# Optimization experiments

Measured on AMD Instinct MI355X. Metric: run time of the kernel, lower is better.

Reference implementation:

```python
import jax, jax.numpy as jnp
import numpy as np

N = 50000          # nodes
E = 400000         # edges
MUL0 = 16          # multiplicity of 0e irreps (node & message)
MUL1 = 8           # multiplicity of 1o irreps
RBF = 8
HID = 64
CUTOFF = 5.0
WNUM = MUL0*MUL0 + MUL1*MUL0 + MUL0*MUL1 + MUL1*MUL1  # 576 tp weights per edge
EPS = 1e-8
INV_SQRT3 = 1.0 / np.sqrt(3.0).astype(np.float32)
A_PATH = 1.0 / np.sqrt(float(MUL0 + MUL1))  # e3nn path normalization (fan_in = 24 for both outputs)


def _split_sv(x):
    # x: [n, 40] -> scalars [n,16], vectors [n,8,3]
    return x[:, :MUL0], x[:, MUL0:].reshape(-1, MUL1, 3)


def _irrep_norm(x):
    # RMS-normalize each irrep block separately (IrrepNorm)
    s, v = _split_sv(x)
    s_rms = jnp.sqrt(jnp.mean(s * s, axis=-1, keepdims=True) + EPS)
    v_rms = jnp.sqrt(jnp.mean(jnp.sum(v * v, axis=-1), axis=-1, keepdims=True) + EPS)
    return jnp.concatenate([s / s_rms, (v / v_rms[:, :, None]).reshape(-1, MUL1 * 3)], axis=-1)


def setup_inputs() -> dict:
    key = jax.random.key(0)
    ks = jax.random.split(key, 20)
    inp = {
        'x': jax.random.normal(ks[0], (N, MUL0 + 3 * MUL1), jnp.float32),
        'edge_src': jax.random.randint(ks[1], (E,), 0, N, jnp.int32),
        'edge_dst': jax.random.randint(ks[2], (E,), 0, N, jnp.int32),
        'edge_sh': jax.random.normal(ks[3], (E, 4), jnp.float32),
        'edge_rbf': jax.random.uniform(ks[4], (E, RBF), jnp.float32),
        'edge_len': jax.random.uniform(ks[5], (E,), jnp.float32) * CUTOFF,
        # radial MLP producing per-edge TP weights
        'w_r1': jax.random.normal(ks[6], (RBF, HID), jnp.float32) / np.sqrt(RBF),
        'b_r1': jnp.zeros((HID,), jnp.float32),
        'w_r2': jax.random.normal(ks[7], (HID, WNUM), jnp.float32) / np.sqrt(HID),
        'b_r2': jnp.zeros((WNUM,), jnp.float32),
        # edge gate MLP
        'w_g1': jax.random.normal(ks[8], (RBF, HID), jnp.float32) / np.sqrt(RBF),
        'b_g1': jnp.zeros((HID,), jnp.float32),
        'w_g2': jax.random.normal(ks[9], (HID, 1), jnp.float32) / np.sqrt(HID),
        'b_g2': jnp.zeros((1,), jnp.float32),
        # msg_linear: 16x0e+8x1o -> (16x0e scalars + 8x0e gates) + 8x1o gated
        'Wm_s': jax.random.normal(ks[10], (MUL0, MUL0 + MUL1), jnp.float32),
        'Wm_v': jax.random.normal(ks[11], (MUL1, MUL1), jnp.float32),
        # update_linear and self_linear: 16x0e+8x1o -> 16x0e+8x1o
        'Wu_s': jax.random.normal(ks[12], (MUL0, MUL0), jnp.float32),
        'Wu_v': jax.random.normal(ks[13], (MUL1, MUL1), jnp.float32),
        'Ws_s': jax.random.normal(ks[14], (MUL0, MUL0), jnp.float32),
        'Ws_v': jax.random.normal(ks[15], (MUL1, MUL1), jnp.float32),
        'res_scale': jnp.asarray(0.1, jnp.float32),
    }
    return inp


def reference(x, edge_src, edge_dst, edge_sh, edge_rbf, edge_len,
              w_r1, b_r1, w_r2, b_r2, w_g1, b_g1, w_g2, b_g2,
              Wm_s, Wm_v, Wu_s, Wu_v, Ws_s, Ws_v, res_scale):
    x_norm = _irrep_norm(x)
    xs, xv = _split_sv(x_norm)

    # per-edge TP weights from radial MLP
    w = jax.nn.silu(edge_rbf @ w_r1 + b_r1) @ w_r2 + b_r2            # [E, 576]
    o = MUL0 * MUL0
    w1 = w[:, :o].reshape(-1, MUL0, MUL0)                            # 0e x 0e -> 0e
    w2 = w[:, o:o + MUL1 * MUL0].reshape(-1, MUL1, MUL0)             # 1o x 1o -> 0e
    o += MUL1 * MUL0
    w3 = w[:, o:o + MUL0 * MUL1].reshape(-1, MUL0, MUL1)             # 0e x 1o -> 1o
    o += MUL0 * MUL1
    w4 = w[:, o:].reshape(-1, MUL1, MUL1)                            # 1o x 0e -> 1o

    # gather per-edge source features
    s_e = xs[edge_src]                                               # [E,16]
    v_e = xv[edge_src]                                               # [E,8,3]
    sh0 = edge_sh[:, :1]                                             # [E,1]
    sh1 = edge_sh[:, 1:4]                                            # [E,3]

    # fully-connected tensor product (CG for l<=1, component norm, path norm)
    m0 = A_PATH * (jnp.einsum('ei,eij->ej', s_e * sh0, w1)
                   + INV_SQRT3 * jnp.einsum('eic,ec,eij->ej', v_e, sh1, w2))   # [E,16]
    m1 = A_PATH * (jnp.einsum('ei,eij,ec->ejc', s_e, w3, sh1)
                   + jnp.einsum('eic,eij->ejc', v_e * sh0[:, :, None], w4))    # [E,8,3]

    # cutoff and sigmoid edge gate
    cw = 0.5 * (jnp.cos(jnp.pi * edge_len / CUTOFF) + 1.0) * (edge_len < CUTOFF)
    gw = jax.nn.sigmoid(jax.nn.silu(edge_rbf @ w_g1 + b_g1) @ w_g2 + b_g2)     # [E,1]
    ew = cw[:, None] * gw                                                      # [E,1]
    m0 = m0 * ew
    m1 = m1 * ew[:, :, None]

    # scatter-add into destination nodes, normalize by total edge weight
    agg0 = jax.ops.segment_sum(m0, edge_dst, num_segments=N)                   # [N,16]
    agg1 = jax.ops.segment_sum(m1.reshape(-1, MUL1 * 3), edge_dst, num_segments=N).reshape(-1, MUL1, 3)
    norm = jax.ops.segment_sum(ew, edge_dst, num_segments=N)                   # [N,1]
    norm = jnp.maximum(norm, EPS)
    agg0 = agg0 / norm
    agg1 = agg1 / norm[:, :, None]

    # msg_linear (equivariant linear, fan-in normalized)
    sc = agg0 @ Wm_s / np.sqrt(MUL0)                                           # [N,24]
    vv = jnp.einsum('nic,ij->njc', agg1, Wm_v) / np.sqrt(MUL1)                 # [N,8,3]

    # gated nonlinearity
    scal = jax.nn.silu(sc[:, :MUL0])
    gates = jax.nn.sigmoid(sc[:, MUL0:])
    vg = vv * gates[:, :, None]

    # update + self interaction, residual
    out_s = scal @ Wu_s / np.sqrt(MUL0) + xs @ Ws_s / np.sqrt(MUL0)
    out_v = (jnp.einsum('nic,ij->njc', vg, Wu_v) + jnp.einsum('nic,ij->njc', xv, Ws_v)) / np.sqrt(MUL1)
    out = jnp.concatenate([out_s, out_v.reshape(-1, MUL1 * 3)], axis=-1)
    return x + res_scale * out
```

## Files before the change

### kernel.cpp

```cpp
#include <hip/hip_runtime.h>
#include <cstdint>

#define MUL0 16
#define MUL1 8
#define NRBF 8
#define HID 64
#define WNUM 576
#define CUTOFF 5.0f
#define EPSF 1e-8f

#define INV_SQRT3 0.57735026918962576f
#define A_PATH    0.20412414523193154f
#define Q16       0.25f
#define Q8        0.35355339059327373f
#define PI_OVER_CUT 0.62831853071795865f

typedef _Float16 f16;
typedef _Float16 f16x8 __attribute__((ext_vector_type(8)));
typedef float f32x4 __attribute__((ext_vector_type(4)));

__device__ __forceinline__ float sigm(float x) { return 1.0f / (1.0f + __expf(-x)); }

extern "C" __global__ __launch_bounds__(256) void k_prep_w2t(
    const float* __restrict__ w_r2, f16* __restrict__ W2T) {
  int t = blockIdx.x * 256 + threadIdx.x;
  if (t >= HID * WNUM) return;
  int n = t >> 6, k = t & 63;
  W2T[n * 64 + k] = (f16)w_r2[k * WNUM + n];
}

extern "C" __global__ __launch_bounds__(64) void k_xnorm(
    const float* __restrict__ x, float* __restrict__ xnorm, int N) {
  int n = blockIdx.x * 64 + threadIdx.x;
  if (n >= N) return;
  const float4* xr = (const float4*)(x + (long long)n * 40);
  float4 vv[10];
#pragma unroll
  for (int i = 0; i < 10; i++) vv[i] = xr[i];
  float* f = (float*)vv;
  float ss = 0.f, vs = 0.f;
#pragma unroll
  for (int i = 0; i < 16; i++) ss += f[i] * f[i];
#pragma unroll
  for (int i = 16; i < 40; i++) vs += f[i] * f[i];
  float sr = rsqrtf(ss * (1.0f / 16.0f) + EPSF);
  float vr = rsqrtf(vs * (1.0f / 8.0f) + EPSF);
#pragma unroll
  for (int i = 0; i < 16; i++) f[i] *= sr;
#pragma unroll
  for (int i = 16; i < 40; i++) f[i] *= vr;
  float4* o = (float4*)(xnorm + (long long)n * 40);
#pragma unroll
  for (int i = 0; i < 10; i++) o[i] = vv[i];
}

extern "C" __global__ __launch_bounds__(256) void k_hist(
    const int* __restrict__ edst, int* __restrict__ hist, int E) {
  int e = blockIdx.x * 256 + threadIdx.x;
  if (e < E) atomicAdd(&hist[edst[e]], 1);
}

extern "C" __global__ __launch_bounds__(256) void k_scan1(
    const int* __restrict__ hist, int* __restrict__ iscan,
    int* __restrict__ bsum, int N) {
  __shared__ int sm[256];
  int i = blockIdx.x * 256 + threadIdx.x;
  int t = threadIdx.x;
  sm[t] = (i < N) ? hist[i] : 0;
  __syncthreads();
#pragma unroll
  for (int d = 1; d < 256; d <<= 1) {
    int add = (t >= d) ? sm[t - d] : 0;
    __syncthreads();
    sm[t] += add;
    __syncthreads();
  }
  if (i < N) iscan[i] = sm[t];
  if (t == 255) bsum[blockIdx.x] = sm[255];
}

extern "C" __global__ __launch_bounds__(256) void k_scan2(
    int* __restrict__ bsum, int nb) {
  __shared__ int sm[256];
  int t = threadIdx.x;
  sm[t] = (t < nb) ? bsum[t] : 0;
  __syncthreads();
#pragma unroll
  for (int d = 1; d < 256; d <<= 1) {
    int add = (t >= d) ? sm[t - d] : 0;
    __syncthreads();
    sm[t] += add;
    __syncthreads();
  }
  if (t < nb) bsum[t] = sm[t];
}

extern "C" __global__ __launch_bounds__(256) void k_scan3(
    const int* __restrict__ hist, const int* __restrict__ iscan,
    const int* __restrict__ bsum, int* __restrict__ cursor, int N) {
  int i = blockIdx.x * 256 + threadIdx.x;
  if (i >= N) return;
  int base = blockIdx.x ? bsum[blockIdx.x - 1] : 0;
  cursor[i] = iscan[i] - hist[i] + base;
}

extern "C" __global__ __launch_bounds__(256) void k_scatter(
    const int* __restrict__ edst, int* __restrict__ cursor,
    int* __restrict__ perm, int E) {
  int e = blockIdx.x * 256 + threadIdx.x;
  if (e >= E) return;
  int p = atomicAdd(&cursor[edst[e]], 1);
  perm[p] = e;
}

extern "C" __global__ __launch_bounds__(256, 3) void k_edge(
    const float* __restrict__ xnorm, const int* __restrict__ perm,
    const int* __restrict__ esrc, const int* __restrict__ edst,
    const float* __restrict__ sh, const float* __restrict__ rbf,
    const float* __restrict__ elen,
    const float* __restrict__ w_r1, const float* __restrict__ b_r1,
    const float* __restrict__ w_g1, const float* __restrict__ b_g1,
    const float* __restrict__ w_g2, const float* __restrict__ b_g2,
    const float* __restrict__ b_r2, const f16* __restrict__ W2T,
    float* __restrict__ agg0, float* __restrict__ agg1,
    float* __restrict__ normb, int E) {
  __shared__ __align__(16) f16   s_H[4][32][72];
  __shared__ __align__(16) float s_sn[4][32][20];
  __shared__ __align__(16) float s_v[4][32][24];
  __shared__ __align__(16) float s_a1[4][32][12];
  __shared__ __align__(16) float s_sh[4][32][4];
  __shared__ __align__(16) float s_rbf[4][32][8];

  const int t = threadIdx.x;
  const int w = t >> 6;
  const int lane = t & 63;
  const long long eb = (long long)blockIdx.x * 128 + w * 32;

  int pl = 0, dstv = 0, srcv = 0;
  float lenv = 1e9f;
  if (lane < 32) {
    long long g2 = eb + lane;
    if (g2 < E) pl = perm[g2];
    srcv = esrc[pl];
    dstv = edst[pl];
    lenv = elen[pl];
    *(float4*)&s_sh[w][lane][0] = *(const float4*)&sh[(long long)pl * 4];
  }
  {
    int e = lane >> 1, half = lane & 1;
    int pe = __shfl(pl, e);
    *(float4*)&s_rbf[w][e][half * 4] =
        *(const float4*)&rbf[(long long)pe * 8 + half * 4];
  }
  __syncthreads();

  {
    const int ge_l = lane >> 2;
    const int part = lane & 3;
#pragma unroll
    for (int g = 0; g < 2; g++) {
      int e = g * 16 + ge_l;
      int srcn = __shfl(srcv, e);
      const float* xr = xnorm + (long long)srcn * 40;
      if (part < 2) {
        float4 aLo = *(const float4*)(xr + part * 8);
        float4 aHi = *(const float4*)(xr + part * 8 + 4);
        *(float4*)&s_sn[w][e][part * 8] = aLo;
        *(float4*)&s_sn[w][e][part * 8 + 4] = aHi;
      } else {
        const int i0 = (part - 2) * 4;
        const float* vp = xr + 16 + i0 * 3;
        float4 v0 = *(const float4*)(vp);
        float4 v1 = *(const float4*)(vp + 4);
        float4 v2 = *(const float4*)(vp + 8);
        *(float4*)&s_v[w][e][i0 * 3] = v0;
        *(float4*)&s_v[w][e][i0 * 3 + 4] = v1;
        *(float4*)&s_v[w][e][i0 * 3 + 8] = v2;
        float4 shq = *(const float4*)&s_sh[w][e][0];
        float s1x = shq.y, s1y = shq.z, s1z = shq.w;
        s_a1[w][e][i0]     = INV_SQRT3 * (v0.x * s1x + v0.y * s1y + v0.z * s1z);
        s_a1[w][e][i0 + 1] = INV_SQRT3 * (v0.w * s1x + v1.x * s1y + v1.y * s1z);
        s_a1[w][e][i0 + 2] = INV_SQRT3 * (v1.z * s1x + v1.w * s1y + v2.x * s1z);
        s_a1[w][e][i0 + 3] = INV_SQRT3 * (v2.y * s1x + v2.z * s1y + v2.w * s1z);
      }
    }
  }

  {
    float wr[8];
#pragma unroll
    for (int r = 0; r < 8; r++) wr[r] = w_r1[r * HID + lane];
    float bh = b_r1[lane];
#pragma unroll 4
    for (int u = 0; u < 32; u++) {
      float4 ra = *(const float4*)&s_rbf[w][u][0];
      float4 rb = *(const float4*)&s_rbf[w][u][4];
      float acc = bh + ra.x * wr[0] + ra.y * wr[1] + ra.z * wr[2] + ra.w * wr[3]
                     + rb.x * wr[4] + rb.y * wr[5] + rb.z * wr[6] + rb.w * wr[7];
      s_H[w][u][lane] = (f16)(acc * sigm(acc));
    }
  }

  float ewv = 0.f;
  {
    const int eg = lane & 31;
    const int hf = lane >> 5;
    float4 ga = *(const float4*)&s_rbf[w][eg][0];
    float4 gb = *(const float4*)&s_rbf[w][eg][4];
    float rv[8] = {ga.x, ga.y, ga.z, ga.w, gb.x, gb.y, gb.z, gb.w};
    float accp = 0.f;
#pragma unroll
    for (int ch = 0; ch < 2; ch++) {
      const int base = hf * 32 + ch * 16;
      float ttv[16];
      {
        const float4 b0 = *(const float4*)&b_g1[base];
        const float4 b1 = *(const float4*)&b_g1[base + 4];
        const float4 b2 = *(const float4*)&b_g1[base + 8];
        const float4 b3 = *(const float4*)&b_g1[base + 12];
        ttv[0] = b0.x; ttv[1] = b0.y; ttv[2] = b0.z; ttv[3] = b0.w;
        ttv[4] = b1.x; ttv[5] = b1.y; ttv[6] = b1.z; ttv[7] = b1.w;
        ttv[8] = b2.x; ttv[9] = b2.y; ttv[10] = b2.z; ttv[11] = b2.w;
        ttv[12] = b3.x; ttv[13] = b3.y; ttv[14] = b3.z; ttv[15] = b3.w;
      }
#pragma unroll
      for (int r = 0; r < 8; r++) {
        const float* wg = w_g1 + r * HID + base;
        float4 w0 = *(const float4*)(wg);
        float4 w1 = *(const float4*)(wg + 4);
        float4 w2 = *(const float4*)(wg + 8);
        float4 w3 = *(const float4*)(wg + 12);
        float rr = rv[r];
        ttv[0] += rr * w0.x; ttv[1] += rr * w0.y; ttv[2] += rr * w0.z; ttv[3] += rr * w0.w;
        ttv[4] += rr * w1.x; ttv[5] += rr * w1.y; ttv[6] += rr * w1.z; ttv[7] += rr * w1.w;
        ttv[8] += rr * w2.x; ttv[9] += rr * w2.y; ttv[10] += rr * w2.z; ttv[11] += rr * w2.w;
        ttv[12] += rr * w3.x; ttv[13] += rr * w3.y; ttv[14] += rr * w3.z; ttv[15] += rr * w3.w;
      }
      const float4 g0 = *(const float4*)&w_g2[base];
      const float4 g1 = *(const float4*)&w_g2[base + 4];
      const float4 g2 = *(const float4*)&w_g2[base + 8];
      const float4 g3 = *(const float4*)&w_g2[base + 12];
      float gw[16] = {g0.x, g0.y, g0.z, g0.w, g1.x, g1.y, g1.z, g1.w,
                      g2.x, g2.y, g2.z, g2.w, g3.x, g3.y, g3.z, g3.w};
#pragma unroll
      for (int k = 0; k < 16; k++) accp += ttv[k] * sigm(ttv[k]) * gw[k];
    }
    accp += __shfl_xor(accp, 32);
    if (lane < 32) {
      long long g2e = eb + lane;
      if (g2e < E) {
        float len = lenv;
        float cw = (len < CUTOFF) ? 0.5f * (__cosf(PI_OVER_CUT * len) + 1.0f) : 0.f;
        ewv = cw * sigm(accp + b_g2[0]);
      }
    }
  }
  __syncthreads();

  const int quad = lane >> 4;
  const int c = lane & 15;

  const f16x8 af00 = *(const f16x8*)&s_H[w][c][quad * 8];
  const f16x8 af01 = *(const f16x8*)&s_H[w][c][32 + quad * 8];
  const f16x8 af10 = *(const f16x8*)&s_H[w][16 + c][quad * 8];
  const f16x8 af11 = *(const f16x8*)&s_H[w][16 + c][32 + quad * 8];

  float p1[2][4] = {{0.f}}, p2[2][4] = {{0.f}}, t3[2][4] = {{0.f}};
  float mx[2][4] = {{0.f}}, my[2][4] = {{0.f}}, mz[2][4] = {{0.f}};

  const f16* wb = W2T + (long long)c * 64 + quad * 8;
  const float* bp = b_r2 + c;

#pragma unroll 2
  for (int jt = 0; jt < 16; jt++) {
    f16x8 b0 = *(const f16x8*)(wb + jt * 1024);
    f16x8 b1 = *(const f16x8*)(wb + jt * 1024 + 32);
    float bias = bp[jt * 16];
    f32x4 C0 = {0.f, 0.f, 0.f, 0.f};
    C0 = __builtin_amdgcn_mfma_f32_16x16x32_f16(af00, b0, C0, 0, 0, 0);
    C0 = __builtin_amdgcn_mfma_f32_16x16x32_f16(af01, b1, C0, 0, 0, 0);
    f32x4 C1 = {0.f, 0.f, 0.f, 0.f};
    C1 = __builtin_amdgcn_mfma_f32_16x16x32_f16(af10, b0, C1, 0, 0, 0);
    C1 = __builtin_amdgcn_mfma_f32_16x16x32_f16(af11, b1, C1, 0, 0, 0);
#pragma unroll
    for (int r = 0; r < 4; r++) {
      p1[0][r] += s_sn[w][quad * 4 + r][jt] * (C0[r] + bias);
      p1[1][r] += s_sn[w][16 + quad * 4 + r][jt] * (C1[r] + bias);
    }
  }
#pragma unroll 2
  for (int jt = 16; jt < 24; jt++) {
    f16x8 b0 = *(const f16x8*)(wb + jt * 1024);
    f16x8 b1 = *(const f16x8*)(wb + jt * 1024 + 32);
    float bias = bp[jt * 16];
    f32x4 C0 = {0.f, 0.f, 0.f, 0.f};
    C0 = __builtin_amdgcn_mfma_f32_16x16x32_f16(af00, b0, C0, 0, 0, 0);
    C0 = __builtin_amdgcn_mfma_f32_16x16x32_f16(af01, b1, C0, 0, 0, 0);
    f32x4 C1 = {0.f, 0.f, 0.f, 0.f};
    C1 = __builtin_amdgcn_mfma_f32_16x16x32_f16(af10, b0, C1, 0, 0, 0);
    C1 = __builtin_amdgcn_mfma_f32_16x16x32_f16(af11, b1, C1, 0, 0, 0);
    const int i = jt - 16;
#pragma unroll
    for (int r = 0; r < 4; r++) {
      p2[0][r] += s_a1[w][quad * 4 + r][i] * (C0[r] + bias);
      p2[1][r] += s_a1[w][16 + quad * 4 + r][i] * (C1[r] + bias);
    }
  }
#pragma unroll 2
  for (int jt = 24; jt < 32; jt++) {
    f16x8 b0 = *(const f16x8*)(wb + jt * 1024);
    f16x8 b1 = *(const f16x8*)(wb + jt * 1024 + 32);
    float bias = bp[jt * 16];
    f32x4 C0 = {0.f, 0.f, 0.f, 0.f};
    C0 = __builtin_amdgcn_mfma_f32_16x16x32_f16(af00, b0, C0, 0, 0, 0);
    C0 = __builtin_amdgcn_mfma_f32_16x16x32_f16(af01, b1, C0, 0, 0, 0);
    f32x4 C1 = {0.f, 0.f, 0.f, 0.f};
    C1 = __builtin_amdgcn_mfma_f32_16x16x32_f16(af10, b0, C1, 0, 0, 0);
    C1 = __builtin_amdgcn_mfma_f32_16x16x32_f16(af11, b1, C1, 0, 0, 0);
    const int i = (jt - 24) * 2 + (c >> 3);
#pragma unroll
    for (int r = 0; r < 4; r++) {
      t3[0][r] += s_sn[w][quad * 4 + r][i] * (C0[r] + bias);
      t3[1][r] += s_sn[w][16 + quad * 4 + r][i] * (C1[r] + bias);
    }
  }
#pragma unroll 2
  for (int jt = 32; jt < 36; jt++) {
    f16x8 b0 = *(const f16x8*)(wb + jt * 1024);
    f16x8 b1 = *(const f16x8*)(wb + jt * 1024 + 32);
    float bias = bp[jt * 16];
    f32x4 C0 = {0.f, 0.f, 0.f, 0.f};
    C0 = __builtin_amdgcn_mfma_f32_16x16x32_f16(af00, b0, C0, 0, 0, 0);
    C0 = __builtin_amdgcn_mfma_f32_16x16x32_f16(af01, b1, C0, 0, 0, 0);
    f32x4 C1 = {0.f, 0.f, 0.f, 0.f};
    C1 = __builtin_amdgcn_mfma_f32_16x16x32_f16(af10, b0, C1, 0, 0, 0);
    C1 = __builtin_amdgcn_mfma_f32_16x16x32_f16(af11, b1, C1, 0, 0, 0);
    const int i = (jt - 32) * 2 + (c >> 3);
#pragma unroll
    for (int r = 0; r < 4; r++) {
      float wv0 = C0[r] + bias;
      float wv1 = C1[r] + bias;
      mx[0][r] += s_v[w][quad * 4 + r][3 * i] * wv0;
      my[0][r] += s_v[w][quad * 4 + r][3 * i + 1] * wv0;
      mz[0][r] += s_v[w][quad * 4 + r][3 * i + 2] * wv0;
      mx[1][r] += s_v[w][16 + quad * 4 + r][3 * i] * wv1;
      my[1][r] += s_v[w][16 + quad * 4 + r][3 * i + 1] * wv1;
      mz[1][r] += s_v[w][16 + quad * 4 + r][3 * i + 2] * wv1;
    }
  }

#pragma unroll
  for (int g = 0; g < 2; g++)
#pragma unroll
    for (int r = 0; r < 4; r++) {
      t3[g][r] += __shfl_xor(t3[g][r], 8);
      mx[g][r] += __shfl_xor(mx[g][r], 8);
      my[g][r] += __shfl_xor(my[g][r], 8);
      mz[g][r] += __shfl_xor(mz[g][r], 8);
    }

#pragma unroll
  for (int g = 0; g < 2; g++) {
    const int e0g = g * 16 + quad * 4;
    int cur = __shfl(dstv, e0g);
    float acc0 = 0.f, a1x = 0.f, a1y = 0.f, a1z = 0.f, nacc = 0.f;
#pragma unroll
    for (int r = 0; r < 4; r++) {
      const int e = e0g + r;
      const int dst = __shfl(dstv, e);
      const float ew = __shfl(ewv, e);
      if (dst != cur) {
        atomicAdd(&agg0[(long long)cur * 16 + c], acc0);
        if (c < 8) {
          long long b = (long long)cur * 24 + (long long)c * 3;
          atomicAdd(&agg1[b], a1x);
          atomicAdd(&agg1[b + 1], a1y);
          atomicAdd(&agg1[b + 2], a1z);
        } else if (c == 8) {
          atomicAdd(&normb[cur], nacc);
        }
        acc0 = a1x = a1y = a1z = nacc = 0.f;
        cur = dst;
      }
      float sc = A_PATH * ew;
      float sh0 = s_sh[w][e][0];
      acc0 += (sh0 * p1[g][r] + p2[g][r]) * sc;
      if (c < 8) {
        float t3v = t3[g][r] * sc;
        float scs = sc * sh0;
        a1x += t3v * s_sh[w][e][1] + mx[g][r] * scs;
        a1y += t3v * s_sh[w][e][2] + my[g][r] * scs;
        a1z += t3v * s_sh[w][e][3] + mz[g][r] * scs;
      } else if (c == 8) {
        nacc += ew;
      }
    }
    atomicAdd(&agg0[(long long)cur * 16 + c], acc0);
    if (c < 8) {
      long long b = (long long)cur * 24 + (long long)c * 3;
      atomicAdd(&agg1[b], a1x);
      atomicAdd(&agg1[b + 1], a1y);
      atomicAdd(&agg1[b + 2], a1z);
    } else if (c == 8) {
      atomicAdd(&normb[cur], nacc);
    }
  }
}

extern "C" __global__ __launch_bounds__(64) void k_node(
    const float* __restrict__ x, const float* __restrict__ xnorm,
    const float* __restrict__ agg0, const float* __restrict__ agg1,
    const float* __restrict__ normb, const float* __restrict__ Wm_s,
    const float* __restrict__ Wm_v, const float* __restrict__ Wu_s,
    const float* __restrict__ Wu_v, const float* __restrict__ Ws_s,
    const float* __restrict__ Ws_v, const float* __restrict__ res_scale_p,
    float* __restrict__ out, int N) {
  __shared__ float sWms[384];
  __shared__ float sWmv[64];
  __shared__ float sWus[256];
  __shared__ float sWuv[64];
  __shared__ float sWss[256];
  __shared__ float sWsv[64];
  int t = threadIdx.x;
  for (int i = t; i < 384; i += 64) sWms[i] = Wm_s[i];
  sWmv[t] = Wm_v[t];
  for (int i = t; i < 256; i += 64) sWus[i] = Wu_s[i];
  sWuv[t] = Wu_v[t];
  for (int i = t; i < 256; i += 64) sWss[i] = Ws_s[i];
  sWsv[t] = Ws_v[t];
  __syncthreads();
  int n = blockIdx.x * 64 + t;
  if (n >= N) return;

  float inv = 1.0f / fmaxf(normb[n], EPSF);
  float4 a04[4], a14[6];
  {
    const float4* p = (const float4*)(agg0 + (long long)n * 16);
#pragma unroll
    for (int i = 0; i < 4; i++) a04[i] = p[i];
    const float4* q = (const float4*)(agg1 + (long long)n * 24);
#pragma unroll
    for (int i = 0; i < 6; i++) a14[i] = q[i];
  }
  float* a0 = (float*)a04;
  float* a1 = (float*)a14;
#pragma unroll
  for (int i = 0; i < 16; i++) a0[i] *= inv;
#pragma unroll
  for (int i = 0; i < 24; i++) a1[i] *= inv;

  float scal[16], gate[8];
#pragma unroll
  for (int jj = 0; jj < 24; jj++) {
    float acc = 0.f;
#pragma unroll
    for (int i = 0; i < 16; i++) acc += a0[i] * sWms[i * 24 + jj];
    acc *= Q16;
    if (jj < 16) scal[jj] = acc * sigm(acc);
    else gate[jj - 16] = sigm(acc);
  }
  float vg[24];
#pragma unroll
  for (int j = 0; j < 8; j++) {
    float g = gate[j];
#pragma unroll
    for (int cc = 0; cc < 3; cc++) {
      float acc = 0.f;
#pragma unroll
      for (int i = 0; i < 8; i++) acc += a1[i * 3 + cc] * sWmv[i * 8 + j];
      vg[j * 3 + cc] = acc * Q8 * g;
    }
  }
  float4 xn4[10], xo4[10];
  {
    const float4* p = (const float4*)(xnorm + (long long)n * 40);
    const float4* q = (const float4*)(x + (long long)n * 40);
#pragma unroll
    for (int i = 0; i < 10; i++) { xn4[i] = p[i]; xo4[i] = q[i]; }
  }
  const float* xn = (const float*)xn4;
  const float* xo = (const float*)xo4;
  float rs = res_scale_p[0];

  float4 ob[10];
  float* ov = (float*)ob;
#pragma unroll
  for (int j = 0; j < 16; j++) {
    float acc = 0.f, acc2 = 0.f;
#pragma unroll
    for (int i = 0; i < 16; i++) {
      acc += scal[i] * sWus[i * 16 + j];
      acc2 += xn[i] * sWss[i * 16 + j];
    }
    ov[j] = xo[j] + rs * ((acc + acc2) * Q16);
  }
#pragma unroll
  for (int j = 0; j < 8; j++) {
#pragma unroll
    for (int cc = 0; cc < 3; cc++) {
      float acc = 0.f;
#pragma unroll
      for (int i = 0; i < 8; i++)
        acc += vg[i * 3 + cc] * sWuv[i * 8 + j] + xn[16 + i * 3 + cc] * sWsv[i * 8 + j];
      ov[16 + j * 3 + cc] = xo[16 + j * 3 + cc] + rs * (acc * Q8);
    }
  }
  float4* po = (float4*)(out + (long long)n * 40);
#pragma unroll
  for (int i = 0; i < 10; i++) po[i] = ob[i];
}

extern "C" void kernel_launch(void* const* d_in, const int* in_sizes, int n_in,
                              void* d_out, int out_size, void* d_ws, size_t ws_size,
                              hipStream_t stream) {
  const float* x = (const float*)d_in[0];
  const int* esrc = (const int*)d_in[1];
  const int* edst = (const int*)d_in[2];
  const float* sh = (const float*)d_in[3];
  const float* rbf = (const float*)d_in[4];
  const float* elen = (const float*)d_in[5];
  const float* w_r1 = (const float*)d_in[6];
  const float* b_r1 = (const float*)d_in[7];
  const float* w_r2 = (const float*)d_in[8];
  const float* b_r2 = (const float*)d_in[9];
  const float* w_g1 = (const float*)d_in[10];
  const float* b_g1 = (const float*)d_in[11];
  const float* w_g2 = (const float*)d_in[12];
  const float* b_g2 = (const float*)d_in[13];
  const float* Wm_s = (const float*)d_in[14];
  const float* Wm_v = (const float*)d_in[15];
  const float* Wu_s = (const float*)d_in[16];
  const float* Wu_v = (const float*)d_in[17];
  const float* Ws_s = (const float*)d_in[18];
  const float* Ws_v = (const float*)d_in[19];
  const float* res_scale = (const float*)d_in[20];

  const int N = in_sizes[0] / 40;
  const int E = in_sizes[1];

  char* ws = (char*)d_ws;
  size_t off = 0;
  float* xnorm = (float*)(ws + off); off += (size_t)N * 40 * sizeof(float);
  off = (off + 255) & ~(size_t)255;
  float* agg0 = (float*)(ws + off); off += (size_t)N * 16 * sizeof(float);
  float* agg1 = (float*)(ws + off); off += (size_t)N * 24 * sizeof(float);
  float* normb = (float*)(ws + off); off += (size_t)N * sizeof(float);
  off = (off + 255) & ~(size_t)255;
  f16* W2T = (f16*)(ws + off); off += (size_t)WNUM * 64 * sizeof(f16);
  off = (off + 255) & ~(size_t)255;
  int* hist   = (int*)(ws + off); off += (size_t)N * sizeof(int);
  int* iscan  = (int*)(ws + off); off += (size_t)N * sizeof(int);
  int* cursor = (int*)(ws + off); off += (size_t)N * sizeof(int);
  int* bsum   = (int*)(ws + off); off += 256 * sizeof(int);
  off = (off + 255) & ~(size_t)255;
  int* perm   = (int*)(ws + off); off += (size_t)E * sizeof(int);

  hipMemsetAsync(agg0, 0, (size_t)N * 41 * sizeof(float), stream);
  hipMemsetAsync(hist, 0, (size_t)N * sizeof(int), stream);

  const int nbE = (E + 255) / 256;
  const int nbN = (N + 255) / 256;

  k_hist<<<nbE, 256, 0, stream>>>(edst, hist, E);
  k_scan1<<<nbN, 256, 0, stream>>>(hist, iscan, bsum, N);
  k_scan2<<<1, 256, 0, stream>>>(bsum, nbN);
  k_scan3<<<nbN, 256, 0, stream>>>(hist, iscan, bsum, cursor, N);
  k_scatter<<<nbE, 256, 0, stream>>>(edst, cursor, perm, E);

  k_prep_w2t<<<(HID * WNUM + 255) / 256, 256, 0, stream>>>(w_r2, W2T);
  k_xnorm<<<(N + 63) / 64, 64, 0, stream>>>(x, xnorm, N);

  int nblk = (E + 127) / 128;
  k_edge<<<nblk, 256, 0, stream>>>(xnorm, perm, esrc, edst, sh, rbf, elen,
                                   w_r1, b_r1, w_g1, b_g1, w_g2, b_g2, b_r2,
                                   W2T, agg0, agg1, normb, E);

  k_node<<<(N + 63) / 64, 64, 0, stream>>>(x, xnorm, agg0, agg1, normb, Wm_s,
                                           Wm_v, Wu_s, Wu_v, Ws_s, Ws_v,
                                           res_scale, (float*)d_out, N);
}
```

Measured before the change: 370.2 us.

## Stage TP weight tiles through double-buffered LDS and fold memsets into kernels

The edge kernel no longer reads W2T fragments straight from global memory in each wave. The block now cooperatively loads 4 KB chunks into a swizzled, double-buffered LDS region that reuses the s_H space once the A fragments are in registers, and the jt loops are fully unrolled through macros. The two hipMemsetAsync calls are removed: hist is zeroed in k_prep_w2t, which now launches first over N, and agg0, agg1 and normb are zeroed in k_xnorm. This cuts launch overhead and repeated global or L2 traffic for weights, at the cost of 17 extra pairs of block-wide barriers in the hot loop.

```diff
diff --git a/kernel.cpp b/kernel.cpp
--- a/kernel.cpp
+++ b/kernel.cpp
@@ -22,15 +22,20 @@
 __device__ __forceinline__ float sigm(float x) { return 1.0f / (1.0f + __expf(-x)); }
 
 extern "C" __global__ __launch_bounds__(256) void k_prep_w2t(
-    const float* __restrict__ w_r2, f16* __restrict__ W2T) {
+    const float* __restrict__ w_r2, f16* __restrict__ W2T,
+    int* __restrict__ hist, int N) {
   int t = blockIdx.x * 256 + threadIdx.x;
-  if (t >= HID * WNUM) return;
-  int n = t >> 6, k = t & 63;
-  W2T[n * 64 + k] = (f16)w_r2[k * WNUM + n];
+  if (t < HID * WNUM) {
+    int n = t >> 6, k = t & 63;
+    W2T[n * 64 + k] = (f16)w_r2[k * WNUM + n];
+  }
+  if (t < N) hist[t] = 0;
 }
 
 extern "C" __global__ __launch_bounds__(64) void k_xnorm(
-    const float* __restrict__ x, float* __restrict__ xnorm, int N) {
+    const float* __restrict__ x, float* __restrict__ xnorm,
+    float* __restrict__ agg0, float* __restrict__ agg1,
+    float* __restrict__ normb, int N) {
   int n = blockIdx.x * 64 + threadIdx.x;
   if (n >= N) return;
   const float4* xr = (const float4*)(x + (long long)n * 40);
@@ -52,6 +57,14 @@
   float4* o = (float4*)(xnorm + (long long)n * 40);
 #pragma unroll
   for (int i = 0; i < 10; i++) o[i] = vv[i];
+  float4 z = {0.f, 0.f, 0.f, 0.f};
+  float4* pa0 = (float4*)(agg0 + (long long)n * 16);
+#pragma unroll
+  for (int i = 0; i < 4; i++) pa0[i] = z;
+  float4* pa1 = (float4*)(agg1 + (long long)n * 24);
+#pragma unroll
+  for (int i = 0; i < 6; i++) pa1[i] = z;
+  normb[n] = 0.f;
 }
 
 extern "C" __global__ __launch_bounds__(256) void k_hist(
@@ -112,6 +125,48 @@
   int p = atomicAdd(&cursor[edst[e]], 1);
   perm[p] = e;
 }
+
+#define MFMA16(a, b, cc) __builtin_amdgcn_mfma_f32_16x16x32_f16(a, b, cc, 0, 0, 0)
+
+#define JT_HEAD(jt) \
+  const char* tb = rb + ((((jt) >> 1) & 1) * 4096) + (((jt) & 1) * 2048); \
+  f16x8 b0 = *(const f16x8*)(tb + cRow + ch0); \
+  f16x8 b1 = *(const f16x8*)(tb + cRow + ch1); \
+  float bias = bp[(jt) * 16]; \
+  f32x4 C0 = {0.f, 0.f, 0.f, 0.f}; \
+  C0 = MFMA16(af00, b0, C0); C0 = MFMA16(af01, b1, C0); \
+  f32x4 C1 = {0.f, 0.f, 0.f, 0.f}; \
+  C1 = MFMA16(af10, b0, C1); C1 = MFMA16(af11, b1, C1);
+
+#define DO_JT1(jt) { JT_HEAD(jt) \
+  _Pragma("unroll") for (int r = 0; r < 4; r++) { \
+    p1[0][r] += s_sn[w][quad * 4 + r][(jt)] * (C0[r] + bias); \
+    p1[1][r] += s_sn[w][16 + quad * 4 + r][(jt)] * (C1[r] + bias); } }
+
+#define DO_JT2(jt) { JT_HEAD(jt) const int i = (jt) - 16; \
+  _Pragma("unroll") for (int r = 0; r < 4; r++) { \
+    p2[0][r] += s_a1[w][quad * 4 + r][i] * (C0[r] + bias); \
+    p2[1][r] += s_a1[w][16 + quad * 4 + r][i] * (C1[r] + bias); } }
+
+#define DO_JT3(jt) { JT_HEAD(jt) const int i = ((jt) - 24) * 2 + (c >> 3); \
+  _Pragma("unroll") for (int r = 0; r < 4; r++) { \
+    t3[0][r] += s_sn[w][quad * 4 + r][i] * (C0[r] + bias); \
+    t3[1][r] += s_sn[w][16 + quad * 4 + r][i] * (C1[r] + bias); } }
+
+#define DO_JT4(jt) { JT_HEAD(jt) const int i = ((jt) - 32) * 2 + (c >> 3); \
+  _Pragma("unroll") for (int r = 0; r < 4; r++) { \
+    float wv0 = C0[r] + bias, wv1 = C1[r] + bias; \
+    mx[0][r] += s_v[w][quad * 4 + r][3 * i] * wv0; \
+    my[0][r] += s_v[w][quad * 4 + r][3 * i + 1] * wv0; \
+    mz[0][r] += s_v[w][quad * 4 + r][3 * i + 2] * wv0; \
+    mx[1][r] += s_v[w][16 + quad * 4 + r][3 * i] * wv1; \
+    my[1][r] += s_v[w][16 + quad * 4 + r][3 * i + 1] * wv1; \
+    mz[1][r] += s_v[w][16 + quad * 4 + r][3 * i + 2] * wv1; } }
+
+#define STAGE(s) { __syncthreads(); \
+  *(uint4*)(rbw + (((s) + 1) & 1) * 4096 + t * 16) = ld; \
+  if ((s) < 16) ld = *(const uint4*)(wsrc + ((s) + 2) * 4096); \
+  __syncthreads(); }
 
 extern "C" __global__ __launch_bounds__(256, 3) void k_edge(
     const float* __restrict__ xnorm, const int* __restrict__ perm,
@@ -124,12 +179,13 @@
     const float* __restrict__ b_r2, const f16* __restrict__ W2T,
     float* __restrict__ agg0, float* __restrict__ agg1,
     float* __restrict__ normb, int E) {
-  __shared__ __align__(16) f16   s_H[4][32][72];
-  __shared__ __align__(16) float s_sn[4][32][20];
-  __shared__ __align__(16) float s_v[4][32][24];
-  __shared__ __align__(16) float s_a1[4][32][12];
-  __shared__ __align__(16) float s_sh[4][32][4];
-  __shared__ __align__(16) float s_rbf[4][32][8];
+  __shared__ __align__(16) char smem[53248];
+  f16   (*s_H)[32][72]  = (f16(*)[32][72])(smem);
+  float (*s_sn)[32][20] = (float(*)[32][20])(smem + 18432);
+  float (*s_v)[32][24]  = (float(*)[32][24])(smem + 28672);
+  float (*s_a1)[32][12] = (float(*)[32][12])(smem + 40960);
+  float (*s_sh)[32][4]  = (float(*)[32][4])(smem + 47104);
+  float (*s_rbf)[32][8] = (float(*)[32][8])(smem + 49152);
 
   const int t = threadIdx.x;
   const int w = t >> 6;
@@ -194,9 +250,9 @@
 #pragma unroll 4
     for (int u = 0; u < 32; u++) {
       float4 ra = *(const float4*)&s_rbf[w][u][0];
-      float4 rb = *(const float4*)&s_rbf[w][u][4];
+      float4 rb2 = *(const float4*)&s_rbf[w][u][4];
       float acc = bh + ra.x * wr[0] + ra.y * wr[1] + ra.z * wr[2] + ra.w * wr[3]
-                     + rb.x * wr[4] + rb.y * wr[5] + rb.z * wr[6] + rb.w * wr[7];
+                     + rb2.x * wr[4] + rb2.y * wr[5] + rb2.z * wr[6] + rb2.w * wr[7];
       s_H[w][u][lane] = (f16)(acc * sigm(acc));
     }
   }
@@ -249,8 +305,7 @@
     if (lane < 32) {
       long long g2e = eb + lane;
       if (g2e < E) {
-        float len = lenv;
-        float cw = (len < CUTOFF) ? 0.5f * (__cosf(PI_OVER_CUT * len) + 1.0f) : 0.f;
+        float cw = (lenv < CUTOFF) ? 0.5f * (__cosf(PI_OVER_CUT * lenv) + 1.0f) : 0.f;
         ewv = cw * sigm(accp + b_g2[0]);
       }
     }
@@ -264,90 +319,47 @@
   const f16x8 af01 = *(const f16x8*)&s_H[w][c][32 + quad * 8];
   const f16x8 af10 = *(const f16x8*)&s_H[w][16 + c][quad * 8];
   const f16x8 af11 = *(const f16x8*)&s_H[w][16 + c][32 + quad * 8];
+  __syncthreads();
+
+  const char* rb = (const char*)smem;
+  char* rbw = (char*)smem;
+  const int stile = t >> 7;
+  const int sc = (t >> 3) & 15;
+  const int sj = t & 7;
+  const char* wsrc = (const char*)W2T + stile * 2048 + sc * 128 +
+                     ((sj ^ (sc & 7)) << 4);
+
+  const int cRow = c * 128;
+  const int ch0 = ((quad ^ (c & 7)) << 4);
+  const int ch1 = (((quad + 4) ^ (c & 7)) << 4);
+
+  uint4 ld = *(const uint4*)(wsrc);
+  *(uint4*)(rbw + t * 16) = ld;
+  ld = *(const uint4*)(wsrc + 4096);
+  __syncthreads();
 
   float p1[2][4] = {{0.f}}, p2[2][4] = {{0.f}}, t3[2][4] = {{0.f}};
   float mx[2][4] = {{0.f}}, my[2][4] = {{0.f}}, mz[2][4] = {{0.f}};
-
-  const f16* wb = W2T + (long long)c * 64 + quad * 8;
   const float* bp = b_r2 + c;
 
-#pragma unroll 2
-  for (int jt = 0; jt < 16; jt++) {
-    f16x8 b0 = *(const f16x8*)(wb + jt * 1024);
-    f16x8 b1 = *(const f16x8*)(wb + jt * 1024 + 32);
-    float bias = bp[jt * 16];
-    f32x4 C0 = {0.f, 0.f, 0.f, 0.f};
-    C0 = __builtin_amdgcn_mfma_f32_16x16x32_f16(af00, b0, C0, 0, 0, 0);
-    C0 = __builtin_amdgcn_mfma_f32_16x16x32_f16(af01, b1, C0, 0, 0, 0);
-    f32x4 C1 = {0.f, 0.f, 0.f, 0.f};
-    C1 = __builtin_amdgcn_mfma_f32_16x16x32_f16(af10, b0, C1, 0, 0, 0);
-    C1 = __builtin_amdgcn_mfma_f32_16x16x32_f16(af11, b1, C1, 0, 0, 0);
-#pragma unroll
-    for (int r = 0; r < 4; r++) {
-      p1[0][r] += s_sn[w][quad * 4 + r][jt] * (C0[r] + bias);
-      p1[1][r] += s_sn[w][16 + quad * 4 + r][jt] * (C1[r] + bias);
-    }
-  }
-#pragma unroll 2
-  for (int jt = 16; jt < 24; jt++) {
-    f16x8 b0 = *(const f16x8*)(wb + jt * 1024);
-    f16x8 b1 = *(const f16x8*)(wb + jt * 1024 + 32);
-    float bias = bp[jt * 16];
-    f32x4 C0 = {0.f, 0.f, 0.f, 0.f};
-    C0 = __builtin_amdgcn_mfma_f32_16x16x32_f16(af00, b0, C0, 0, 0, 0);
-    C0 = __builtin_amdgcn_mfma_f32_16x16x32_f16(af01, b1, C0, 0, 0, 0);
-    f32x4 C1 = {0.f, 0.f, 0.f, 0.f};
-    C1 = __builtin_amdgcn_mfma_f32_16x16x32_f16(af10, b0, C1, 0, 0, 0);
-    C1 = __builtin_amdgcn_mfma_f32_16x16x32_f16(af11, b1, C1, 0, 0, 0);
-    const int i = jt - 16;
-#pragma unroll
-    for (int r = 0; r < 4; r++) {
-      p2[0][r] += s_a1[w][quad * 4 + r][i] * (C0[r] + bias);
-      p2[1][r] += s_a1[w][16 + quad * 4 + r][i] * (C1[r] + bias);
-    }
-  }
-#pragma unroll 2
-  for (int jt = 24; jt < 32; jt++) {
-    f16x8 b0 = *(const f16x8*)(wb + jt * 1024);
-    f16x8 b1 = *(const f16x8*)(wb + jt * 1024 + 32);
-    float bias = bp[jt * 16];
-    f32x4 C0 = {0.f, 0.f, 0.f, 0.f};
-    C0 = __builtin_amdgcn_mfma_f32_16x16x32_f16(af00, b0, C0, 0, 0, 0);
-    C0 = __builtin_amdgcn_mfma_f32_16x16x32_f16(af01, b1, C0, 0, 0, 0);
-    f32x4 C1 = {0.f, 0.f, 0.f, 0.f};
-    C1 = __builtin_amdgcn_mfma_f32_16x16x32_f16(af10, b0, C1, 0, 0, 0);
-    C1 = __builtin_amdgcn_mfma_f32_16x16x32_f16(af11, b1, C1, 0, 0, 0);
-    const int i = (jt - 24) * 2 + (c >> 3);
-#pragma unroll
-    for (int r = 0; r < 4; r++) {
-      t3[0][r] += s_sn[w][quad * 4 + r][i] * (C0[r] + bias);
-      t3[1][r] += s_sn[w][16 + quad * 4 + r][i] * (C1[r] + bias);
-    }
-  }
-#pragma unroll 2
-  for (int jt = 32; jt < 36; jt++) {
-    f16x8 b0 = *(const f16x8*)(wb + jt * 1024);
-    f16x8 b1 = *(const f16x8*)(wb + jt * 1024 + 32);
-    float bias = bp[jt * 16];
-    f32x4 C0 = {0.f, 0.f, 0.f, 0.f};
-    C0 = __builtin_amdgcn_mfma_f32_16x16x32_f16(af00, b0, C0, 0, 0, 0);
-    C0 = __builtin_amdgcn_mfma_f32_16x16x32_f16(af01, b1, C0, 0, 0, 0);
-    f32x4 C1 = {0.f, 0.f, 0.f, 0.f};
-    C1 = __builtin_amdgcn_mfma_f32_16x16x32_f16(af10, b0, C1, 0, 0, 0);
-    C1 = __builtin_amdgcn_mfma_f32_16x16x32_f16(af11, b1, C1, 0, 0, 0);
-    const int i = (jt - 32) * 2 + (c >> 3);
-#pragma unroll
-    for (int r = 0; r < 4; r++) {
-      float wv0 = C0[r] + bias;
-      float wv1 = C1[r] + bias;
-      mx[0][r] += s_v[w][quad * 4 + r][3 * i] * wv0;
-      my[0][r] += s_v[w][quad * 4 + r][3 * i + 1] * wv0;
-      mz[0][r] += s_v[w][quad * 4 + r][3 * i + 2] * wv0;
-      mx[1][r] += s_v[w][16 + quad * 4 + r][3 * i] * wv1;
-      my[1][r] += s_v[w][16 + quad * 4 + r][3 * i + 1] * wv1;
-      mz[1][r] += s_v[w][16 + quad * 4 + r][3 * i + 2] * wv1;
-    }
-  }
+  DO_JT1(0)  DO_JT1(1)  STAGE(0)
+  DO_JT1(2)  DO_JT1(3)  STAGE(1)
+  DO_JT1(4)  DO_JT1(5)  STAGE(2)
+  DO_JT1(6)  DO_JT1(7)  STAGE(3)
+  DO_JT1(8)  DO_JT1(9)  STAGE(4)
+  DO_JT1(10) DO_JT1(11) STAGE(5)
+  DO_JT1(12) DO_JT1(13) STAGE(6)
+  DO_JT1(14) DO_JT1(15) STAGE(7)
+  DO_JT2(16) DO_JT2(17) STAGE(8)
+  DO_JT2(18) DO_JT2(19) STAGE(9)
+  DO_JT2(20) DO_JT2(21) STAGE(10)
+  DO_JT2(22) DO_JT2(23) STAGE(11)
+  DO_JT3(24) DO_JT3(25) STAGE(12)
+  DO_JT3(26) DO_JT3(27) STAGE(13)
+  DO_JT3(28) DO_JT3(29) STAGE(14)
+  DO_JT3(30) DO_JT3(31) STAGE(15)
+  DO_JT4(32) DO_JT4(33) STAGE(16)
+  DO_JT4(34) DO_JT4(35)
 
 #pragma unroll
   for (int g = 0; g < 2; g++)
@@ -382,12 +394,12 @@
         acc0 = a1x = a1y = a1z = nacc = 0.f;
         cur = dst;
       }
-      float sc = A_PATH * ew;
+      float sc2 = A_PATH * ew;
       float sh0 = s_sh[w][e][0];
-      acc0 += (sh0 * p1[g][r] + p2[g][r]) * sc;
+      acc0 += (sh0 * p1[g][r] + p2[g][r]) * sc2;
       if (c < 8) {
-        float t3v = t3[g][r] * sc;
-        float scs = sc * sh0;
+        float t3v = t3[g][r] * sc2;
+        float scs = sc2 * sh0;
         a1x += t3v * s_sh[w][e][1] + mx[g][r] * scs;
         a1y += t3v * s_sh[w][e][2] + my[g][r] * scs;
         a1z += t3v * s_sh[w][e][3] + mz[g][r] * scs;
@@ -555,20 +567,17 @@
   off = (off + 255) & ~(size_t)255;
   int* perm   = (int*)(ws + off); off += (size_t)E * sizeof(int);
 
-  hipMemsetAsync(agg0, 0, (size_t)N * 41 * sizeof(float), stream);
-  hipMemsetAsync(hist, 0, (size_t)N * sizeof(int), stream);
-
   const int nbE = (E + 255) / 256;
   const int nbN = (N + 255) / 256;
 
+  k_prep_w2t<<<nbN, 256, 0, stream>>>(w_r2, W2T, hist, N);
   k_hist<<<nbE, 256, 0, stream>>>(edst, hist, E);
   k_scan1<<<nbN, 256, 0, stream>>>(hist, iscan, bsum, N);
   k_scan2<<<1, 256, 0, stream>>>(bsum, nbN);
   k_scan3<<<nbN, 256, 0, stream>>>(hist, iscan, bsum, cursor, N);
   k_scatter<<<nbE, 256, 0, stream>>>(edst, cursor, perm, E);
 
-  k_prep_w2t<<<(HID * WNUM + 255) / 256, 256, 0, stream>>>(w_r2, W2T);
-  k_xnorm<<<(N + 63) / 64, 64, 0, stream>>>(x, xnorm, N);
+  k_xnorm<<<(N + 63) / 64, 64, 0, stream>>>(x, xnorm, agg0, agg1, normb, N);
 
   int nblk = (E + 127) / 128;
   k_edge<<<nblk, 256, 0, stream>>>(xnorm, perm, esrc, edst, sh, rbf, elen,
```

Result: slower. 1.002 ms (+170.7%).

## Fold buffer zeroing into prep kernels, pad s_v, deepen MFMA loop unroll

Applied to the files above, without the earlier changes.

Removes the two hipMemsetAsync calls. The hist clear is folded into k_prep_w2t, which is now launched first over N-sized blocks. Zeroing of agg0/agg1/normb moves into k_xnorm. It also pads the s_v shared array row to 26 floats, likely to reduce LDS bank conflicts, and raises the unroll of the MFMA weight loops from 2 to 4. The unroll may increase register pressure under launch_bounds(256,3). k_prep_w2t grid is nbN (≈196 blocks ≈ 50176 threads), which covers HID*WNUM=36864, so correctness holds.

```diff
diff --git a/kernel.cpp b/kernel.cpp
--- a/kernel.cpp
+++ b/kernel.cpp
@@ -22,15 +22,20 @@
 __device__ __forceinline__ float sigm(float x) { return 1.0f / (1.0f + __expf(-x)); }
 
 extern "C" __global__ __launch_bounds__(256) void k_prep_w2t(
-    const float* __restrict__ w_r2, f16* __restrict__ W2T) {
+    const float* __restrict__ w_r2, f16* __restrict__ W2T,
+    int* __restrict__ hist, int N) {
   int t = blockIdx.x * 256 + threadIdx.x;
-  if (t >= HID * WNUM) return;
-  int n = t >> 6, k = t & 63;
-  W2T[n * 64 + k] = (f16)w_r2[k * WNUM + n];
+  if (t < HID * WNUM) {
+    int n = t >> 6, k = t & 63;
+    W2T[n * 64 + k] = (f16)w_r2[k * WNUM + n];
+  }
+  if (t < N) hist[t] = 0;
 }
 
 extern "C" __global__ __launch_bounds__(64) void k_xnorm(
-    const float* __restrict__ x, float* __restrict__ xnorm, int N) {
+    const float* __restrict__ x, float* __restrict__ xnorm,
+    float* __restrict__ agg0, float* __restrict__ agg1,
+    float* __restrict__ normb, int N) {
   int n = blockIdx.x * 64 + threadIdx.x;
   if (n >= N) return;
   const float4* xr = (const float4*)(x + (long long)n * 40);
@@ -52,6 +57,14 @@
   float4* o = (float4*)(xnorm + (long long)n * 40);
 #pragma unroll
   for (int i = 0; i < 10; i++) o[i] = vv[i];
+  float4 z = {0.f, 0.f, 0.f, 0.f};
+  float4* pa0 = (float4*)(agg0 + (long long)n * 16);
+#pragma unroll
+  for (int i = 0; i < 4; i++) pa0[i] = z;
+  float4* pa1 = (float4*)(agg1 + (long long)n * 24);
+#pragma unroll
+  for (int i = 0; i < 6; i++) pa1[i] = z;
+  normb[n] = 0.f;
 }
 
 extern "C" __global__ __launch_bounds__(256) void k_hist(
@@ -126,7 +139,7 @@
     float* __restrict__ normb, int E) {
   __shared__ __align__(16) f16   s_H[4][32][72];
   __shared__ __align__(16) float s_sn[4][32][20];
-  __shared__ __align__(16) float s_v[4][32][24];
+  __shared__ __align__(16) float s_v[4][32][26];
   __shared__ __align__(16) float s_a1[4][32][12];
   __shared__ __align__(16) float s_sh[4][32][4];
   __shared__ __align__(16) float s_rbf[4][32][8];
@@ -194,9 +207,9 @@
 #pragma unroll 4
     for (int u = 0; u < 32; u++) {
       float4 ra = *(const float4*)&s_rbf[w][u][0];
-      float4 rb = *(const float4*)&s_rbf[w][u][4];
+      float4 rb2 = *(const float4*)&s_rbf[w][u][4];
       float acc = bh + ra.x * wr[0] + ra.y * wr[1] + ra.z * wr[2] + ra.w * wr[3]
-                     + rb.x * wr[4] + rb.y * wr[5] + rb.z * wr[6] + rb.w * wr[7];
+                     + rb2.x * wr[4] + rb2.y * wr[5] + rb2.z * wr[6] + rb2.w * wr[7];
       s_H[w][u][lane] = (f16)(acc * sigm(acc));
     }
   }
@@ -249,8 +262,7 @@
     if (lane < 32) {
       long long g2e = eb + lane;
       if (g2e < E) {
-        float len = lenv;
-        float cw = (len < CUTOFF) ? 0.5f * (__cosf(PI_OVER_CUT * len) + 1.0f) : 0.f;
+        float cw = (lenv < CUTOFF) ? 0.5f * (__cosf(PI_OVER_CUT * lenv) + 1.0f) : 0.f;
         ewv = cw * sigm(accp + b_g2[0]);
       }
     }
@@ -271,7 +283,7 @@
   const f16* wb = W2T + (long long)c * 64 + quad * 8;
   const float* bp = b_r2 + c;
 
-#pragma unroll 2
+#pragma unroll 4
   for (int jt = 0; jt < 16; jt++) {
     f16x8 b0 = *(const f16x8*)(wb + jt * 1024);
     f16x8 b1 = *(const f16x8*)(wb + jt * 1024 + 32);
@@ -288,7 +300,7 @@
       p1[1][r] += s_sn[w][16 + quad * 4 + r][jt] * (C1[r] + bias);
     }
   }
-#pragma unroll 2
+#pragma unroll 4
   for (int jt = 16; jt < 24; jt++) {
     f16x8 b0 = *(const f16x8*)(wb + jt * 1024);
     f16x8 b1 = *(const f16x8*)(wb + jt * 1024 + 32);
@@ -306,7 +318,7 @@
       p2[1][r] += s_a1[w][16 + quad * 4 + r][i] * (C1[r] + bias);
     }
   }
-#pragma unroll 2
+#pragma unroll 4
   for (int jt = 24; jt < 32; jt++) {
     f16x8 b0 = *(const f16x8*)(wb + jt * 1024);
     f16x8 b1 = *(const f16x8*)(wb + jt * 1024 + 32);
@@ -324,7 +336,7 @@
       t3[1][r] += s_sn[w][16 + quad * 4 + r][i] * (C1[r] + bias);
     }
   }
-#pragma unroll 2
+#pragma unroll 4
   for (int jt = 32; jt < 36; jt++) {
     f16x8 b0 = *(const f16x8*)(wb + jt * 1024);
     f16x8 b1 = *(const f16x8*)(wb + jt * 1024 + 32);
@@ -382,12 +394,12 @@
         acc0 = a1x = a1y = a1z = nacc = 0.f;
         cur = dst;
       }
-      float sc = A_PATH * ew;
+      float sc2 = A_PATH * ew;
       float sh0 = s_sh[w][e][0];
-      acc0 += (sh0 * p1[g][r] + p2[g][r]) * sc;
+      acc0 += (sh0 * p1[g][r] + p2[g][r]) * sc2;
       if (c < 8) {
-        float t3v = t3[g][r] * sc;
-        float scs = sc * sh0;
+        float t3v = t3[g][r] * sc2;
+        float scs = sc2 * sh0;
         a1x += t3v * s_sh[w][e][1] + mx[g][r] * scs;
         a1y += t3v * s_sh[w][e][2] + my[g][r] * scs;
         a1z += t3v * s_sh[w][e][3] + mz[g][r] * scs;
@@ -555,20 +567,17 @@
   off = (off + 255) & ~(size_t)255;
   int* perm   = (int*)(ws + off); off += (size_t)E * sizeof(int);
 
-  hipMemsetAsync(agg0, 0, (size_t)N * 41 * sizeof(float), stream);
-  hipMemsetAsync(hist, 0, (size_t)N * sizeof(int), stream);
-
   const int nbE = (E + 255) / 256;
   const int nbN = (N + 255) / 256;
 
+  k_prep_w2t<<<nbN, 256, 0, stream>>>(w_r2, W2T, hist, N);
   k_hist<<<nbE, 256, 0, stream>>>(edst, hist, E);
   k_scan1<<<nbN, 256, 0, stream>>>(hist, iscan, bsum, N);
   k_scan2<<<1, 256, 0, stream>>>(bsum, nbN);
   k_scan3<<<nbN, 256, 0, stream>>>(hist, iscan, bsum, cursor, N);
   k_scatter<<<nbE, 256, 0, stream>>>(edst, cursor, perm, E);
 
-  k_prep_w2t<<<(HID * WNUM + 255) / 256, 256, 0, stream>>>(w_r2, W2T);
-  k_xnorm<<<(N + 63) / 64, 64, 0, stream>>>(x, xnorm, N);
+  k_xnorm<<<(N + 63) / 64, 64, 0, stream>>>(x, xnorm, agg0, agg1, normb, N);
 
   int nblk = (E + 127) / 128;
   k_edge<<<nblk, 256, 0, stream>>>(xnorm, perm, esrc, edst, sh, rbf, elen,
```

New measurement: 386.8 us. 1.04x slower.
